# Optimization experiments

Hardware: AMD Instinct MI355X
Metric: run time of the kernel (lower is better)

Reference implementation:

```python
import jax, jax.numpy as jnp
import numpy as np


def setup_inputs() -> dict:
    key = jax.random.key(0)
    k1, k2 = jax.random.split(key)
    x = jax.random.normal(k1, (16, 512, 4096), dtype=jnp.float32)      # [N, C_in, L]
    weight = jax.random.normal(k2, (512, 512, 3), dtype=jnp.float32)   # [C_out, C_in, K]
    scale = jnp.ones((1,), dtype=jnp.float32)                           # learned scalar
    return {"x": x, "weight": weight, "scale": scale}


def reference(x, weight, scale):
    EPS = 1e-5
    # per-sample activation scale over (C, L), clamped
    x_scale = jnp.clip(jnp.mean(jnp.abs(x), axis=(1, 2), keepdims=True), EPS)  # [N,1,1]
    x_norm = x / x_scale
    # straight-through binarization: forward sign(w), backward identity
    w_bin = jax.lax.stop_gradient(jnp.sign(weight)) + weight - jax.lax.stop_gradient(weight)
    w_scale = jnp.mean(jnp.abs(weight))  # scalar
    # conv1d, stride=1, padding=1, dilation=1, groups=1  ->  output [N, C_out, L]
    out = jax.lax.conv_general_dilated(
        x_norm, w_bin,
        window_strides=(1,),
        padding=[(1, 1)],
        dimension_numbers=("NCH", "OIH", "NCH"),
    )
    return out * w_scale * x_scale * scale
```

## Files before the change

kernel.cpp:

```cpp
#include <hip/hip_runtime.h>
#include <stdint.h>


#define CIN   512
#define COUT  512
#define LLEN  4096
#define NBAT  16
#define KW    3
#define WELEMS (COUT*CIN*KW)

typedef __bf16 bf16x8 __attribute__((ext_vector_type(8)));
typedef float  f32x4  __attribute__((ext_vector_type(4)));

__device__ __forceinline__ uint32_t f2bf(float f) {
    union { float f; uint32_t u; } v; v.f = f;
    return (v.u + 0x7fffu + ((v.u >> 16) & 1u)) >> 16;
}

__global__ __launch_bounds__(256) void pack_w(const float* __restrict__ w,
                                              unsigned short* __restrict__ wsw,
                                              float* __restrict__ partial) {
    __shared__ float red[256];
    int tid = threadIdx.x;
    int idx = blockIdx.x * 256 + tid;
    float s = 0.f;
    int co = idx >> 9, ci = idx & 511;
#pragma unroll
    for (int t = 0; t < KW; ++t) {
        float v = w[idx * 3 + t];
        s += fabsf(v);
        unsigned short b = (v > 0.f) ? 0x3F80 : ((v < 0.f) ? 0xBF80 : 0);
        wsw[((t * 64 + (ci >> 3)) * 512 + co) * 8 + (ci & 7)] = b;
    }
    red[tid] = s;
    __syncthreads();
    for (int off = 128; off > 0; off >>= 1) {
        if (tid < off) red[tid] += red[tid + off];
        __syncthreads();
    }
    if (tid == 0) partial[blockIdx.x] = red[0];
}

__global__ __launch_bounds__(256) void wscale_final(const float* __restrict__ partial,
                                                    const float* __restrict__ scale,
                                                    float* __restrict__ fac) {
    __shared__ float red[256];
    int tid = threadIdx.x;
    red[tid] = partial[tid] + partial[tid + 256] + partial[tid + 512] + partial[tid + 768];
    __syncthreads();
    for (int off = 128; off > 0; off >>= 1) {
        if (tid < off) red[tid] += red[tid + off];
        __syncthreads();
    }
    if (tid == 0) fac[0] = red[0] * (1.0f / (float)WELEMS) * scale[0];
}

__global__ __launch_bounds__(256, 2) void conv_mfma(const float* __restrict__ x,
                                                    const unsigned short* __restrict__ wsw,
                                                    const float* __restrict__ fac,
                                                    float* __restrict__ out) {
    int swz = (blockIdx.x & 7) * 256 + (blockIdx.x >> 3);
    int cob = swz & 3;
    int lb  = (swz >> 2) & 31;
    int n   = swz >> 7;
    int co0 = cob * 128;
    int l0  = lb * 128;

    __shared__ char Bs[2][8320];

    int tid  = threadIdx.x;
    int wave = tid >> 6;
    int lane = tid & 63;
    int wco  = (wave >> 1) * 64;
    int wl   = (wave & 1) * 64;
    int m    = lane & 15;
    int ks   = lane >> 4;
    const int p  = tid & 15;
    const int fb = tid >> 4;

    const float* xbase = x + (size_t)(n * 512) * LLEN;
    const char*  wb    = (const char*)wsw;

    int aoff[4];
#pragma unroll
    for (int ms = 0; ms < 4; ++ms)
        aoff[ms] = ks * 8192 + (co0 + wco + ms * 16 + m) * 16;

    float4 b0[2], b1[2];
    float  hReg = 0.f;

    auto LOADB = [&](int c) {
        const float* xrow0 = xbase + (size_t)(c * 32 + 2 * p) * LLEN + l0;
        const float* xrow1 = xrow0 + LLEN;
        b0[0] = reinterpret_cast<const float4*>(xrow0)[fb];
        b1[0] = reinterpret_cast<const float4*>(xrow1)[fb];
        b0[1] = reinterpret_cast<const float4*>(xrow0)[fb + 16];
        b1[1] = reinterpret_cast<const float4*>(xrow1)[fb + 16];
        if (tid < 32)
            hReg = (l0 > 0) ? xbase[(size_t)(c * 32 + tid) * LLEN + l0 - 1] : 0.f;
        else if (tid < 64)
            hReg = (l0 + 128 < LLEN) ? xbase[(size_t)(c * 32 + tid - 32) * LLEN + l0 + 128] : 0.f;
    };
    auto WRITEB = [&](char* BsD) {
        int kslot = p >> 2, jj = (2 * p) & 7;
#pragma unroll
        for (int half = 0; half < 2; ++half) {
#pragma unroll
            for (int e = 0; e < 4; ++e) {
                int ll = (fb + half * 16) * 4 + 1 + e;
                uint32_t pk = f2bf(((const float*)&b0[half])[e])
                            | (f2bf(((const float*)&b1[half])[e]) << 16);
                *reinterpret_cast<uint32_t*>(
                    BsD + ll * 64 + ((kslot ^ ((ll >> 1) & 3)) << 4) + jj * 2) = pk;
            }
        }
        if (tid < 32) {
            *reinterpret_cast<unsigned short*>(
                BsD + ((tid >> 3) << 4) + (tid & 7) * 2) = (unsigned short)f2bf(hReg);
        } else if (tid < 64) {
            int ci = tid - 32, ll = 129;
            *reinterpret_cast<unsigned short*>(
                BsD + ll * 64 + (((ci >> 3) ^ ((ll >> 1) & 3)) << 4) + (ci & 7) * 2)
                = (unsigned short)f2bf(hReg);
        }
    };

    f32x4 acc[4][4];
#pragma unroll
    for (int i = 0; i < 4; ++i)
#pragma unroll
        for (int j = 0; j < 4; ++j) acc[i][j] = (f32x4){0.f, 0.f, 0.f, 0.f};

    LOADB(0);
    WRITEB(Bs[0]);
    __syncthreads();

    int cur = 0;
    for (int c = 0; c < 16; ++c) {
        bf16x8 afr[KW][4];
        {
            const char* ab = wb + c * 32768;
#pragma unroll
            for (int t = 0; t < KW; ++t)
#pragma unroll
                for (int ms = 0; ms < 4; ++ms)
                    afr[t][ms] = *reinterpret_cast<const bf16x8*>(
                        ab + t * 524288 + aoff[ms]);
        }
        __builtin_amdgcn_sched_barrier(0);
        if (c < 15) LOADB(c + 1);

        const char* Bc = Bs[cur];
#pragma unroll
        for (int t = 0; t < KW; ++t) {
            bf16x8 bfr[4];
#pragma unroll
            for (int ns = 0; ns < 4; ++ns) {
                int ll = wl + ns * 16 + m + t;
                bfr[ns] = *reinterpret_cast<const bf16x8*>(
                    Bc + ll * 64 + ((ks ^ ((ll >> 1) & 3)) << 4));
            }
#pragma unroll
            for (int ms = 0; ms < 4; ++ms)
#pragma unroll
                for (int ns = 0; ns < 4; ++ns)
                    acc[ms][ns] = __builtin_amdgcn_mfma_f32_16x16x32_bf16(
                        afr[t][ms], bfr[ns], acc[ms][ns], 0, 0, 0);
        }

        if (c < 15) {
            asm volatile("s_waitcnt vmcnt(0)" ::: "memory");
            WRITEB(Bs[cur ^ 1]);
            asm volatile("s_waitcnt lgkmcnt(0)" ::: "memory");
            __builtin_amdgcn_s_barrier();
        }
        cur ^= 1;
    }

    float fscale = fac[0];
    int r4 = (lane >> 4) * 4;
#pragma unroll
    for (int ms = 0; ms < 4; ++ms) {
#pragma unroll
        for (int ns = 0; ns < 4; ++ns) {
            int col  = l0 + wl + ns * 16 + m;
            int row0 = co0 + wco + ms * 16 + r4;
            float* o = out + ((size_t)(n * 512 + row0)) * LLEN + col;
#pragma unroll
            for (int r = 0; r < 4; ++r)
                o[(size_t)r * LLEN] = acc[ms][ns][r] * fscale;
        }
    }
}

extern "C" void kernel_launch(void* const* d_in, const int* in_sizes, int n_in,
                              void* d_out, int out_size, void* d_ws, size_t ws_size,
                              hipStream_t stream) {
    const float* x     = (const float*)d_in[0];
    const float* w     = (const float*)d_in[1];
    const float* scale = (const float*)d_in[2];
    float* out = (float*)d_out;

    float* partials = (float*)d_ws;
    float* fac      = (float*)((char*)d_ws + 4096);
    unsigned short* wsw = (unsigned short*)((char*)d_ws + 8192);

    pack_w<<<(COUT * CIN) / 256, 256, 0, stream>>>(w, wsw, partials);
    wscale_final<<<1, 256, 0, stream>>>(partials, scale, fac);
    conv_mfma<<<NBAT * 4 * 32, 256, 0, stream>>>(x, wsw, fac, out);
}
```

Measured before the change: 141.3 us.

## Stage full input-channel slab in LDS once, retile to 256x64 output blocks

Each block now loads and converts its whole 512-channel by 66-position input window into a 66 KB LDS buffer up front, then runs all 16 channel chunks without per-chunk reloads or barriers. The output tile changes from 128 channels x 128 positions to 256 channels x 64 positions, with each wave owning 64 output channels. Weight fragments are now loaded per tap inside the loop. The aim is to drop the double-buffered pipeline's per-chunk barriers and to read each x element only twice instead of four times. The cost is that the large LDS footprint cuts occupancy, and the global x loads are no longer overlapped with MFMA work.

```diff
diff --git a/kernel.cpp b/kernel.cpp
--- a/kernel.cpp
+++ b/kernel.cpp
@@ -60,70 +60,51 @@
                                                     const float* __restrict__ fac,
                                                     float* __restrict__ out) {
     int swz = (blockIdx.x & 7) * 256 + (blockIdx.x >> 3);
-    int cob = swz & 3;
-    int lb  = (swz >> 2) & 31;
+    int cob = swz & 1;
+    int lb  = (swz >> 1) & 63;
     int n   = swz >> 7;
-    int co0 = cob * 128;
-    int l0  = lb * 128;
+    int co0 = cob * 256;
+    int l0  = lb * 64;
 
-    __shared__ char Bs[2][8320];
+    __shared__ char Bs[66 * 1024];
 
     int tid  = threadIdx.x;
     int wave = tid >> 6;
     int lane = tid & 63;
-    int wco  = (wave >> 1) * 64;
-    int wl   = (wave & 1) * 64;
     int m    = lane & 15;
     int ks   = lane >> 4;
-    const int p  = tid & 15;
-    const int fb = tid >> 4;
 
-    const float* xbase = x + (size_t)(n * 512) * LLEN;
-    const char*  wb    = (const char*)wsw;
+    {
+        const float* r0 = x + ((size_t)(n * 512 + 2 * tid)) * LLEN + l0;
+        const float* r1 = r0 + LLEN;
+        int sbase = ((tid >> 2) << 4) | ((tid & 3) << 2);
+#pragma unroll 4
+        for (int q = 0; q < 16; ++q) {
+            float4 a = reinterpret_cast<const float4*>(r0)[q];
+            float4 b = reinterpret_cast<const float4*>(r1)[q];
+#pragma unroll
+            for (int e = 0; e < 4; ++e) {
+                int ll = q * 4 + e + 1;
+                uint32_t pk = f2bf(((const float*)&a)[e])
+                            | (f2bf(((const float*)&b)[e]) << 16);
+                int off = ll * 1024 + ((((tid >> 2) ^ (ll & 7)) << 4) | ((tid & 3) << 2));
+                *reinterpret_cast<uint32_t*>(Bs + off) = pk;
+            }
+        }
+        float lo0 = 0.f, lo1 = 0.f, hi0 = 0.f, hi1 = 0.f;
+        if (l0 > 0)            { lo0 = r0[-1]; lo1 = r1[-1]; }
+        if (l0 + 64 < LLEN)    { hi0 = r0[64]; hi1 = r1[64]; }
+        *reinterpret_cast<uint32_t*>(Bs + sbase) = f2bf(lo0) | (f2bf(lo1) << 16);
+        *reinterpret_cast<uint32_t*>(Bs + 65 * 1024
+            + ((((tid >> 2) ^ 1) << 4) | ((tid & 3) << 2))) = f2bf(hi0) | (f2bf(hi1) << 16);
+    }
+    __syncthreads();
 
+    const char* wb = (const char*)wsw;
     int aoff[4];
 #pragma unroll
     for (int ms = 0; ms < 4; ++ms)
-        aoff[ms] = ks * 8192 + (co0 + wco + ms * 16 + m) * 16;
-
-    float4 b0[2], b1[2];
-    float  hReg = 0.f;
-
-    auto LOADB = [&](int c) {
-        const float* xrow0 = xbase + (size_t)(c * 32 + 2 * p) * LLEN + l0;
-        const float* xrow1 = xrow0 + LLEN;
-        b0[0] = reinterpret_cast<const float4*>(xrow0)[fb];
-        b1[0] = reinterpret_cast<const float4*>(xrow1)[fb];
-        b0[1] = reinterpret_cast<const float4*>(xrow0)[fb + 16];
-        b1[1] = reinterpret_cast<const float4*>(xrow1)[fb + 16];
-        if (tid < 32)
-            hReg = (l0 > 0) ? xbase[(size_t)(c * 32 + tid) * LLEN + l0 - 1] : 0.f;
-        else if (tid < 64)
-            hReg = (l0 + 128 < LLEN) ? xbase[(size_t)(c * 32 + tid - 32) * LLEN + l0 + 128] : 0.f;
-    };
-    auto WRITEB = [&](char* BsD) {
-        int kslot = p >> 2, jj = (2 * p) & 7;
-#pragma unroll
-        for (int half = 0; half < 2; ++half) {
-#pragma unroll
-            for (int e = 0; e < 4; ++e) {
-                int ll = (fb + half * 16) * 4 + 1 + e;
-                uint32_t pk = f2bf(((const float*)&b0[half])[e])
-                            | (f2bf(((const float*)&b1[half])[e]) << 16);
-                *reinterpret_cast<uint32_t*>(
-                    BsD + ll * 64 + ((kslot ^ ((ll >> 1) & 3)) << 4) + jj * 2) = pk;
-            }
-        }
-        if (tid < 32) {
-            *reinterpret_cast<unsigned short*>(
-                BsD + ((tid >> 3) << 4) + (tid & 7) * 2) = (unsigned short)f2bf(hReg);
-        } else if (tid < 64) {
-            int ci = tid - 32, ll = 129;
-            *reinterpret_cast<unsigned short*>(
-                BsD + ll * 64 + (((ci >> 3) ^ ((ll >> 1) & 3)) << 4) + (ci & 7) * 2)
-                = (unsigned short)f2bf(hReg);
-        }
-    };
+        aoff[ms] = ks * 8192 + (co0 + wave * 64 + ms * 16 + m) * 16;
 
     f32x4 acc[4][4];
 #pragma unroll
@@ -131,50 +112,28 @@
 #pragma unroll
         for (int j = 0; j < 4; ++j) acc[i][j] = (f32x4){0.f, 0.f, 0.f, 0.f};
 
-    LOADB(0);
-    WRITEB(Bs[0]);
-    __syncthreads();
-
-    int cur = 0;
+#pragma unroll 2
     for (int c = 0; c < 16; ++c) {
-        bf16x8 afr[KW][4];
-        {
-            const char* ab = wb + c * 32768;
-#pragma unroll
-            for (int t = 0; t < KW; ++t)
-#pragma unroll
-                for (int ms = 0; ms < 4; ++ms)
-                    afr[t][ms] = *reinterpret_cast<const bf16x8*>(
-                        ab + t * 524288 + aoff[ms]);
-        }
-        __builtin_amdgcn_sched_barrier(0);
-        if (c < 15) LOADB(c + 1);
-
-        const char* Bc = Bs[cur];
 #pragma unroll
         for (int t = 0; t < KW; ++t) {
-            bf16x8 bfr[4];
+            bf16x8 afr[4], bfr[4];
+#pragma unroll
+            for (int ms = 0; ms < 4; ++ms)
+                afr[ms] = *reinterpret_cast<const bf16x8*>(
+                    wb + t * 524288 + c * 32768 + aoff[ms]);
 #pragma unroll
             for (int ns = 0; ns < 4; ++ns) {
-                int ll = wl + ns * 16 + m + t;
+                int ll = ns * 16 + m + t;
                 bfr[ns] = *reinterpret_cast<const bf16x8*>(
-                    Bc + ll * 64 + ((ks ^ ((ll >> 1) & 3)) << 4));
+                    Bs + ll * 1024 + (((c * 4 + ks) ^ (ll & 7)) << 4));
             }
 #pragma unroll
             for (int ms = 0; ms < 4; ++ms)
 #pragma unroll
                 for (int ns = 0; ns < 4; ++ns)
                     acc[ms][ns] = __builtin_amdgcn_mfma_f32_16x16x32_bf16(
-                        afr[t][ms], bfr[ns], acc[ms][ns], 0, 0, 0);
+                        afr[ms], bfr[ns], acc[ms][ns], 0, 0, 0);
         }
-
-        if (c < 15) {
-            asm volatile("s_waitcnt vmcnt(0)" ::: "memory");
-            WRITEB(Bs[cur ^ 1]);
-            asm volatile("s_waitcnt lgkmcnt(0)" ::: "memory");
-            __builtin_amdgcn_s_barrier();
-        }
-        cur ^= 1;
     }
 
     float fscale = fac[0];
@@ -183,8 +142,8 @@
     for (int ms = 0; ms < 4; ++ms) {
 #pragma unroll
         for (int ns = 0; ns < 4; ++ns) {
-            int col  = l0 + wl + ns * 16 + m;
-            int row0 = co0 + wco + ms * 16 + r4;
+            int col  = l0 + ns * 16 + m;
+            int row0 = co0 + wave * 64 + ms * 16 + r4;
             float* o = out + ((size_t)(n * 512 + row0)) * LLEN + col;
 #pragma unroll
             for (int r = 0; r < 4; ++r)
@@ -207,5 +166,5 @@
 
     pack_w<<<(COUT * CIN) / 256, 256, 0, stream>>>(w, wsw, partials);
     wscale_final<<<1, 256, 0, stream>>>(partials, scale, fac);
-    conv_mfma<<<NBAT * 4 * 32, 256, 0, stream>>>(x, wsw, fac, out);
+    conv_mfma<<<NBAT * 2 * 64, 256, 0, stream>>>(x, wsw, fac, out);
 }
```

Measured after the change: 188.3 us. 1.33x slower.

## Stage binarized weight tiles in LDS via async global-to-LDS DMA double buffer

Applied to the files above, without the earlier changes.

Weight fragments were loaded per wave directly from global memory into registers each chunk. They are now copied block-wide into a double-buffered LDS tile with global_load_lds and prefetched one chunk ahead alongside the activation loads. This removes duplicate global reads across waves and register pressure from holding all three taps. It costs 48KB extra LDS per block and adds LDS reads that may hit bank conflicts.

```diff
diff --git a/kernel.cpp b/kernel.cpp
--- a/kernel.cpp
+++ b/kernel.cpp
@@ -11,6 +11,10 @@
 
 typedef __bf16 bf16x8 __attribute__((ext_vector_type(8)));
 typedef float  f32x4  __attribute__((ext_vector_type(4)));
+
+#define DMA16(g, l) __builtin_amdgcn_global_load_lds( \
+    (const __attribute__((address_space(1))) uint32_t*)(g), \
+    (__attribute__((address_space(3))) uint32_t*)(l), 16, 0, 0)
 
 __device__ __forceinline__ uint32_t f2bf(float f) {
     union { float f; uint32_t u; } v; v.f = f;
@@ -66,6 +70,7 @@
     int co0 = cob * 128;
     int l0  = lb * 128;
 
+    __shared__ char As[2][24576];
     __shared__ char Bs[2][8320];
 
     int tid  = threadIdx.x;
@@ -81,14 +86,20 @@
     const float* xbase = x + (size_t)(n * 512) * LLEN;
     const char*  wb    = (const char*)wsw;
 
-    int aoff[4];
-#pragma unroll
-    for (int ms = 0; ms < 4; ++ms)
-        aoff[ms] = ks * 8192 + (co0 + wco + ms * 16 + m) * 16;
+    auto DMAA = [&](int c, char* Ad) {
+#pragma unroll
+        for (int it = 0; it < 6; ++it) {
+            int g = it * 256 + tid;
+            int s = g >> 7;
+            int r = g & 127;
+            const char* src = wb +
+                ((((s >> 2) * 64 + c * 4 + (s & 3)) * 512) + (co0 + r)) * 16;
+            DMA16(src, Ad + g * 16);
+        }
+    };
 
     float4 b0[2], b1[2];
     float  hReg = 0.f;
-
     auto LOADB = [&](int c) {
         const float* xrow0 = xbase + (size_t)(c * 32 + 2 * p) * LLEN + l0;
         const float* xrow1 = xrow0 + LLEN;
@@ -131,29 +142,28 @@
 #pragma unroll
         for (int j = 0; j < 4; ++j) acc[i][j] = (f32x4){0.f, 0.f, 0.f, 0.f};
 
+    DMAA(0, As[0]);
     LOADB(0);
     WRITEB(Bs[0]);
+    asm volatile("s_waitcnt vmcnt(0)" ::: "memory");
     __syncthreads();
 
-    int cur = 0;
     for (int c = 0; c < 16; ++c) {
-        bf16x8 afr[KW][4];
-        {
-            const char* ab = wb + c * 32768;
-#pragma unroll
-            for (int t = 0; t < KW; ++t)
-#pragma unroll
-                for (int ms = 0; ms < 4; ++ms)
-                    afr[t][ms] = *reinterpret_cast<const bf16x8*>(
-                        ab + t * 524288 + aoff[ms]);
+        if (c < 15) {
+            DMAA(c + 1, As[(c + 1) & 1]);
+            LOADB(c + 1);
         }
         __builtin_amdgcn_sched_barrier(0);
-        if (c < 15) LOADB(c + 1);
-
-        const char* Bc = Bs[cur];
+
+        const char* Ac = As[c & 1];
+        const char* Bc = Bs[c & 1];
 #pragma unroll
         for (int t = 0; t < KW; ++t) {
-            bf16x8 bfr[4];
+            bf16x8 afr[4], bfr[4];
+#pragma unroll
+            for (int ms = 0; ms < 4; ++ms)
+                afr[ms] = *reinterpret_cast<const bf16x8*>(
+                    Ac + ((t * 4 + ks) * 128 + wco + ms * 16 + m) * 16);
 #pragma unroll
             for (int ns = 0; ns < 4; ++ns) {
                 int ll = wl + ns * 16 + m + t;
@@ -165,16 +175,16 @@
 #pragma unroll
                 for (int ns = 0; ns < 4; ++ns)
                     acc[ms][ns] = __builtin_amdgcn_mfma_f32_16x16x32_bf16(
-                        afr[t][ms], bfr[ns], acc[ms][ns], 0, 0, 0);
+                        afr[ms], bfr[ns], acc[ms][ns], 0, 0, 0);
         }
 
         if (c < 15) {
             asm volatile("s_waitcnt vmcnt(0)" ::: "memory");
-            WRITEB(Bs[cur ^ 1]);
+            WRITEB(Bs[(c + 1) & 1]);
             asm volatile("s_waitcnt lgkmcnt(0)" ::: "memory");
             __builtin_amdgcn_s_barrier();
-        }
-        cur ^= 1;
+            __builtin_amdgcn_sched_barrier(0);
+        }
     }
 
     float fscale = fac[0];
```

After: 148.4 us. +5.0%, slower.

## Cover all output channels per block with 512-thread blocks to reuse staged inputs

Applied to the files above, without the earlier changes.

Each block now handles all 512 output channels for a 128-wide L tile, using 8 waves with each wave owning 128 channels by 64 positions. The converted bf16 input tile is therefore loaded and converted once instead of four times across channel blocks. Weight fragments are now loaded per tap inside the loop rather than all up front. The explicit vmcnt wait before the LDS write is removed, and the block swizzle is dropped. This doubles the accumulator registers per thread (128 floats) and leaves only 512 blocks, which risks register pressure, lower occupancy and poorer tail balance.

```diff
diff --git a/kernel.cpp b/kernel.cpp
--- a/kernel.cpp
+++ b/kernel.cpp
@@ -55,15 +55,13 @@
     if (tid == 0) fac[0] = red[0] * (1.0f / (float)WELEMS) * scale[0];
 }
 
-__global__ __launch_bounds__(256, 2) void conv_mfma(const float* __restrict__ x,
+__global__ __launch_bounds__(512, 2) void conv_mfma(const float* __restrict__ x,
                                                     const unsigned short* __restrict__ wsw,
                                                     const float* __restrict__ fac,
                                                     float* __restrict__ out) {
-    int swz = (blockIdx.x & 7) * 256 + (blockIdx.x >> 3);
-    int cob = swz & 3;
-    int lb  = (swz >> 2) & 31;
-    int n   = swz >> 7;
-    int co0 = cob * 128;
+    int bid = blockIdx.x;
+    int lb  = bid & 31;
+    int n   = bid >> 5;
     int l0  = lb * 128;
 
     __shared__ char Bs[2][8320];
@@ -71,63 +69,57 @@
     int tid  = threadIdx.x;
     int wave = tid >> 6;
     int lane = tid & 63;
-    int wco  = (wave >> 1) * 64;
+    int wco  = (wave >> 1) * 128;
     int wl   = (wave & 1) * 64;
     int m    = lane & 15;
     int ks   = lane >> 4;
     const int p  = tid & 15;
-    const int fb = tid >> 4;
+    const int fc = tid >> 4;
 
     const float* xbase = x + (size_t)(n * 512) * LLEN;
     const char*  wb    = (const char*)wsw;
 
-    int aoff[4];
+    int aoff[8];
 #pragma unroll
-    for (int ms = 0; ms < 4; ++ms)
-        aoff[ms] = ks * 8192 + (co0 + wco + ms * 16 + m) * 16;
+    for (int ms = 0; ms < 8; ++ms)
+        aoff[ms] = ks * 8192 + (wco + ms * 16 + m) * 16;
 
-    float4 b0[2], b1[2];
+    float4 b0, b1;
     float  hReg = 0.f;
 
     auto LOADB = [&](int c) {
         const float* xrow0 = xbase + (size_t)(c * 32 + 2 * p) * LLEN + l0;
-        const float* xrow1 = xrow0 + LLEN;
-        b0[0] = reinterpret_cast<const float4*>(xrow0)[fb];
-        b1[0] = reinterpret_cast<const float4*>(xrow1)[fb];
-        b0[1] = reinterpret_cast<const float4*>(xrow0)[fb + 16];
-        b1[1] = reinterpret_cast<const float4*>(xrow1)[fb + 16];
+        b0 = reinterpret_cast<const float4*>(xrow0)[fc];
+        b1 = reinterpret_cast<const float4*>(xrow0 + LLEN)[fc];
         if (tid < 32)
             hReg = (l0 > 0) ? xbase[(size_t)(c * 32 + tid) * LLEN + l0 - 1] : 0.f;
         else if (tid < 64)
             hReg = (l0 + 128 < LLEN) ? xbase[(size_t)(c * 32 + tid - 32) * LLEN + l0 + 128] : 0.f;
     };
-    auto WRITEB = [&](char* BsD) {
+    auto WRITEB = [&](char* d) {
         int kslot = p >> 2, jj = (2 * p) & 7;
 #pragma unroll
-        for (int half = 0; half < 2; ++half) {
-#pragma unroll
-            for (int e = 0; e < 4; ++e) {
-                int ll = (fb + half * 16) * 4 + 1 + e;
-                uint32_t pk = f2bf(((const float*)&b0[half])[e])
-                            | (f2bf(((const float*)&b1[half])[e]) << 16);
-                *reinterpret_cast<uint32_t*>(
-                    BsD + ll * 64 + ((kslot ^ ((ll >> 1) & 3)) << 4) + jj * 2) = pk;
-            }
+        for (int e = 0; e < 4; ++e) {
+            int ll = fc * 4 + 1 + e;
+            uint32_t pk = f2bf(((const float*)&b0)[e])
+                        | (f2bf(((const float*)&b1)[e]) << 16);
+            *reinterpret_cast<uint32_t*>(
+                d + ll * 64 + ((kslot ^ ((ll >> 1) & 3)) << 4) + jj * 2) = pk;
         }
         if (tid < 32) {
             *reinterpret_cast<unsigned short*>(
-                BsD + ((tid >> 3) << 4) + (tid & 7) * 2) = (unsigned short)f2bf(hReg);
+                d + ((tid >> 3) << 4) + (tid & 7) * 2) = (unsigned short)f2bf(hReg);
         } else if (tid < 64) {
             int ci = tid - 32, ll = 129;
             *reinterpret_cast<unsigned short*>(
-                BsD + ll * 64 + (((ci >> 3) ^ ((ll >> 1) & 3)) << 4) + (ci & 7) * 2)
+                d + ll * 64 + (((ci >> 3) ^ ((ll >> 1) & 3)) << 4) + (ci & 7) * 2)
                 = (unsigned short)f2bf(hReg);
         }
     };
 
-    f32x4 acc[4][4];
+    f32x4 acc[8][4];
 #pragma unroll
-    for (int i = 0; i < 4; ++i)
+    for (int i = 0; i < 8; ++i)
 #pragma unroll
         for (int j = 0; j < 4; ++j) acc[i][j] = (f32x4){0.f, 0.f, 0.f, 0.f};
 
@@ -135,25 +127,18 @@
     WRITEB(Bs[0]);
     __syncthreads();
 
-    int cur = 0;
     for (int c = 0; c < 16; ++c) {
-        bf16x8 afr[KW][4];
-        {
-            const char* ab = wb + c * 32768;
-#pragma unroll
-            for (int t = 0; t < KW; ++t)
-#pragma unroll
-                for (int ms = 0; ms < 4; ++ms)
-                    afr[t][ms] = *reinterpret_cast<const bf16x8*>(
-                        ab + t * 524288 + aoff[ms]);
-        }
+        if (c < 15) LOADB(c + 1);
         __builtin_amdgcn_sched_barrier(0);
-        if (c < 15) LOADB(c + 1);
 
-        const char* Bc = Bs[cur];
+        const char* Bc = Bs[c & 1];
 #pragma unroll
         for (int t = 0; t < KW; ++t) {
-            bf16x8 bfr[4];
+            bf16x8 afr[8], bfr[4];
+            const char* ab = wb + t * 524288 + c * 32768;
+#pragma unroll
+            for (int ms = 0; ms < 8; ++ms)
+                afr[ms] = *reinterpret_cast<const bf16x8*>(ab + aoff[ms]);
 #pragma unroll
             for (int ns = 0; ns < 4; ++ns) {
                 int ll = wl + ns * 16 + m + t;
@@ -161,30 +146,29 @@
                     Bc + ll * 64 + ((ks ^ ((ll >> 1) & 3)) << 4));
             }
 #pragma unroll
-            for (int ms = 0; ms < 4; ++ms)
+            for (int ms = 0; ms < 8; ++ms)
 #pragma unroll
                 for (int ns = 0; ns < 4; ++ns)
                     acc[ms][ns] = __builtin_amdgcn_mfma_f32_16x16x32_bf16(
-                        afr[t][ms], bfr[ns], acc[ms][ns], 0, 0, 0);
+                        afr[ms], bfr[ns], acc[ms][ns], 0, 0, 0);
         }
 
         if (c < 15) {
-            asm volatile("s_waitcnt vmcnt(0)" ::: "memory");
-            WRITEB(Bs[cur ^ 1]);
+            WRITEB(Bs[(c + 1) & 1]);
             asm volatile("s_waitcnt lgkmcnt(0)" ::: "memory");
             __builtin_amdgcn_s_barrier();
+            __builtin_amdgcn_sched_barrier(0);
         }
-        cur ^= 1;
     }
 
     float fscale = fac[0];
-    int r4 = (lane >> 4) * 4;
+    int r4 = ks * 4;
 #pragma unroll
-    for (int ms = 0; ms < 4; ++ms) {
+    for (int ms = 0; ms < 8; ++ms) {
 #pragma unroll
         for (int ns = 0; ns < 4; ++ns) {
             int col  = l0 + wl + ns * 16 + m;
-            int row0 = co0 + wco + ms * 16 + r4;
+            int row0 = wco + ms * 16 + r4;
             float* o = out + ((size_t)(n * 512 + row0)) * LLEN + col;
 #pragma unroll
             for (int r = 0; r < 4; ++r)
@@ -207,5 +191,5 @@
 
     pack_w<<<(COUT * CIN) / 256, 256, 0, stream>>>(w, wsw, partials);
     wscale_final<<<1, 256, 0, stream>>>(partials, scale, fac);
-    conv_mfma<<<NBAT * 4 * 32, 256, 0, stream>>>(x, wsw, fac, out);
+    conv_mfma<<<NBAT * 32, 512, 0, stream>>>(x, wsw, fac, out);
 }
```

Measured after the change: 167.8 us. +18.7%, slower.
